# Kernel tuning notes

Measured on AMD Instinct MI355X. Metric: run time of the kernel, lower is better.

## Reference

```python
import jax, jax.numpy as jnp
import numpy as np

HIDDEN = 4096
RANK = 4
DELTA = 1.0
BATCH = 4096


def glorot(key, shape):
    return jax.random.uniform(key, shape, minval=-1.0, maxval=1.0) * jnp.sqrt(2.0 / sum(shape))


def setup_inputs() -> dict:
    key = jax.random.key(0)
    k1, k2, k3, k4, k5, k6 = jax.random.split(key, 6)
    return {
        "h": jax.random.normal(k5, (BATCH, HIDDEN), dtype=jnp.float32),
        "x": jax.random.normal(k6, (BATCH, HIDDEN), dtype=jnp.float32),
        "a_diag": glorot(k1, (HIDDEN,)),
        "p_vec": glorot(k2, (HIDDEN, RANK)),
        "q_vec": glorot(k3, (HIDDEN, RANK)),
        "b_mat": glorot(k4, (HIDDEN, HIDDEN)),
    }


def reference(h, x, a_diag, p_vec, q_vec, b_mat):
    # Per-sample original math: (I + delta*(diag(a) + p q^T)) @ h + delta * b_mat.T @ x
    # Batched (rows of h/x are samples) with the Woodbury-style low-rank form:
    #   A_disc @ h  ->  h + delta*(a*h + (h @ q) @ p^T)
    #   B_disc^T @ x -> delta * (x @ b_mat)
    Ah = h + DELTA * (h * a_diag + (h @ q_vec) @ p_vec.T)  # [B, N]
    Bx = DELTA * (x @ b_mat)                               # [B, N]
    return Ah + Bx
```

## Files before the change

### kernel.cpp

```cpp
#include <hip/hip_runtime.h>
#include <hip/hip_bf16.h>
#include <stdint.h>
#include <stddef.h>

#define HIDDEN 4096
#define BATCH  4096
#define RANK   4

typedef _Float16 f16;
typedef __attribute__((ext_vector_type(8))) _Float16 half8;
typedef __attribute__((ext_vector_type(4))) float f32x4;
typedef __attribute__((ext_vector_type(8))) unsigned short ushort8;

#define ASYNC_COPY16(g, l)                                                     \
  __builtin_amdgcn_global_load_lds(                                            \
      (__attribute__((address_space(1))) void*)(g),                            \
      (__attribute__((address_space(3))) void*)(l), 16, 0, 0)

__global__ void cast_f16_kernel(const float* __restrict__ src, f16* __restrict__ dst) {
  size_t i = ((size_t)blockIdx.x * blockDim.x + threadIdx.x) * 8;
  float4 v0 = *(const float4*)(src + i);
  float4 v1 = *(const float4*)(src + i + 4);
  union { f16 h[8]; ushort8 v; } u;
  u.h[0] = (f16)v0.x; u.h[1] = (f16)v0.y; u.h[2] = (f16)v0.z; u.h[3] = (f16)v0.w;
  u.h[4] = (f16)v1.x; u.h[5] = (f16)v1.y; u.h[6] = (f16)v1.z; u.h[7] = (f16)v1.w;
  *(ushort8*)(dst + i) = u.v;
}

__global__ void transpose_cast_kernel(const float* __restrict__ B, f16* __restrict__ Bt) {
  __shared__ f16 tile[64][80];
  const int t = threadIdx.x;
  const int bx = blockIdx.x;
  const int by = blockIdx.y;
  const int tx = t & 15, ty = t >> 4;
  #pragma unroll
  for (int i = 0; i < 4; i++) {
    int row = ty + i * 16;
    float4 v = *(const float4*)(B + (size_t)(by * 64 + row) * HIDDEN + bx * 64 + tx * 4);
    tile[tx * 4 + 0][row] = (f16)v.x;
    tile[tx * 4 + 1][row] = (f16)v.y;
    tile[tx * 4 + 2][row] = (f16)v.z;
    tile[tx * 4 + 3][row] = (f16)v.w;
  }
  __syncthreads();
  const int wx = t & 7, wy = t >> 3;
  #pragma unroll
  for (int i = 0; i < 2; i++) {
    int n = wy + i * 32;
    ushort8 v = *(ushort8*)&tile[n][wx * 8];
    *(ushort8*)(Bt + (size_t)(bx * 64 + n) * HIDDEN + by * 64 + wx * 8) = v;
  }
}

__global__ void hq_kernel(const float* __restrict__ h, const float* __restrict__ q,
                          float* __restrict__ hq) {
  const int b = blockIdx.x;
  const float* hrow = h + (size_t)b * HIDDEN;
  float a0 = 0.f, a1 = 0.f, a2 = 0.f, a3 = 0.f;
  for (int k = threadIdx.x; k < HIDDEN; k += 256) {
    float hv = hrow[k];
    float4 qv = *(const float4*)(q + (size_t)k * RANK);
    a0 += hv * qv.x; a1 += hv * qv.y; a2 += hv * qv.z; a3 += hv * qv.w;
  }
  #pragma unroll
  for (int off = 32; off; off >>= 1) {
    a0 += __shfl_down(a0, off, 64);
    a1 += __shfl_down(a1, off, 64);
    a2 += __shfl_down(a2, off, 64);
    a3 += __shfl_down(a3, off, 64);
  }
  __shared__ float red[4][4];
  const int wave = threadIdx.x >> 6, lane = threadIdx.x & 63;
  if (lane == 0) { red[wave][0] = a0; red[wave][1] = a1; red[wave][2] = a2; red[wave][3] = a3; }
  __syncthreads();
  if (threadIdx.x < 4) {
    float s = red[0][threadIdx.x] + red[1][threadIdx.x] + red[2][threadIdx.x] + red[3][threadIdx.x];
    hq[(size_t)b * RANK + threadIdx.x] = s;
  }
}

#define BM 128
#define BN 128
#define BK 64

__global__ __launch_bounds__(256) void gemm_fused_kernel(
    const f16* __restrict__ Xb, const f16* __restrict__ Bt,
    const float* __restrict__ h, const float* __restrict__ a_diag,
    const float* __restrict__ p_vec, const float* __restrict__ hq,
    float* __restrict__ out) {
  __shared__ f16 As[BM * BK];
  __shared__ f16 Bs[BN * BK];
  const int tid = threadIdx.x;
  const int bm = blockIdx.x, bn = blockIdx.y;
  const int wave = tid >> 6, lane = tid & 63;
  const int wm = wave & 1, wn = wave >> 1;

  const int srow = tid >> 3;
  const int sseg = (tid & 7) ^ (srow & 7);
  const f16* ag = Xb + (size_t)(bm * BM + srow) * HIDDEN + sseg * 8;
  const f16* bg = Bt + (size_t)(bn * BN + srow) * HIDDEN + sseg * 8;
  char* as_base = (char*)As + wave * 1024;
  char* bs_base = (char*)Bs + wave * 1024;
  const size_t rowblk = (size_t)32 * HIDDEN;

  f32x4 acc[4][4];
  #pragma unroll
  for (int i = 0; i < 4; i++)
    #pragma unroll
    for (int j = 0; j < 4; j++)
      acc[i][j] = (f32x4){0.f, 0.f, 0.f, 0.f};

  const int q = lane >> 4;
  const int fm = lane & 15;
  const int swz = lane & 7;

  for (int k0 = 0; k0 < HIDDEN; k0 += BK) {
    #pragma unroll
    for (int o = 0; o < 4; o++) {
      ASYNC_COPY16(ag + o * rowblk, as_base + o * 4096);
      ASYNC_COPY16(bg + o * rowblk, bs_base + o * 4096);
    }
    ag += BK; bg += BK;
    __syncthreads();

    #pragma unroll
    for (int kk = 0; kk < 2; kk++) {
      const int sa = ((kk << 2) | q) ^ swz;
      half8 af[4], bf[4];
      #pragma unroll
      for (int i = 0; i < 4; i++)
        af[i] = *(const half8*)(As + (wm * 64 + i * 16 + fm) * BK + sa * 8);
      #pragma unroll
      for (int j = 0; j < 4; j++)
        bf[j] = *(const half8*)(Bs + (wn * 64 + j * 16 + fm) * BK + sa * 8);
      #pragma unroll
      for (int i = 0; i < 4; i++)
        #pragma unroll
        for (int j = 0; j < 4; j++)
          acc[i][j] = __builtin_amdgcn_mfma_f32_16x16x32_f16(af[i], bf[j], acc[i][j], 0, 0, 0);
    }
    __syncthreads();
  }

  float ad[4];
  float4 pv[4];
  #pragma unroll
  for (int j = 0; j < 4; j++) {
    const int gn = bn * BN + wn * 64 + j * 16 + fm;
    ad[j] = 1.0f + a_diag[gn];
    pv[j] = *(const float4*)(p_vec + (size_t)gn * RANK);
  }
  #pragma unroll
  for (int i = 0; i < 4; i++) {
    #pragma unroll
    for (int r = 0; r < 4; r++) {
      const size_t gb = (size_t)(bm * BM + wm * 64 + i * 16 + q * 4 + r);
      const float4 hv = *(const float4*)(hq + gb * RANK);
      const size_t rowoff = gb * HIDDEN + bn * BN + wn * 64 + fm;
      #pragma unroll
      for (int j = 0; j < 4; j++) {
        const size_t idx = rowoff + j * 16;
        const float hval = __builtin_nontemporal_load(&h[idx]);
        const float v = acc[i][j][r] + hval * ad[j] +
                        hv.x * pv[j].x + hv.y * pv[j].y + hv.z * pv[j].z + hv.w * pv[j].w;
        __builtin_nontemporal_store(v, &out[idx]);
      }
    }
  }
}

__global__ void gemm_f32_fallback_kernel(const float* __restrict__ x, const float* __restrict__ bmat,
                                         const float* __restrict__ h, const float* __restrict__ a_diag,
                                         const float* __restrict__ p_vec, const float* __restrict__ hq,
                                         float* __restrict__ out) {
  __shared__ float As[16][64];
  __shared__ float Bs[16][68];
  const int t = threadIdx.x;
  const int bx = blockIdx.x, by = blockIdx.y;
  const int tm = t & 15, tn = t >> 4;
  float acc[4][4] = {{0.f}};
  for (int k0 = 0; k0 < HIDDEN; k0 += 16) {
    #pragma unroll
    for (int l = 0; l < 4; l++) {
      int idx = t + l * 256;
      int r = idx >> 4, k = idx & 15;
      As[k][r] = x[(size_t)(by * 64 + r) * HIDDEN + k0 + k];
      int kb = idx >> 6, nb = idx & 63;
      Bs[kb][nb] = bmat[(size_t)(k0 + kb) * HIDDEN + bx * 64 + nb];
    }
    __syncthreads();
    #pragma unroll
    for (int k = 0; k < 16; k++) {
      float av[4], bv[4];
      #pragma unroll
      for (int ii = 0; ii < 4; ii++) av[ii] = As[k][tm * 4 + ii];
      #pragma unroll
      for (int jj = 0; jj < 4; jj++) bv[jj] = Bs[k][tn * 4 + jj];
      #pragma unroll
      for (int ii = 0; ii < 4; ii++)
        #pragma unroll
        for (int jj = 0; jj < 4; jj++)
          acc[ii][jj] += av[ii] * bv[jj];
    }
    __syncthreads();
  }
  #pragma unroll
  for (int jj = 0; jj < 4; jj++) {
    int gn = bx * 64 + tn * 4 + jj;
    float ad = 1.0f + a_diag[gn];
    float4 pv = *(const float4*)(p_vec + (size_t)gn * RANK);
    #pragma unroll
    for (int ii = 0; ii < 4; ii++) {
      size_t gb = (size_t)(by * 64 + tm * 4 + ii);
      float4 hv = *(const float4*)(hq + gb * RANK);
      size_t idx = gb * HIDDEN + gn;
      out[idx] = acc[ii][jj] + h[idx] * ad +
                 hv.x * pv.x + hv.y * pv.y + hv.z * pv.z + hv.w * pv.w;
    }
  }
}

extern "C" void kernel_launch(void* const* d_in, const int* in_sizes, int n_in,
                              void* d_out, int out_size, void* d_ws, size_t ws_size,
                              hipStream_t stream) {
  const float* h      = (const float*)d_in[0];
  const float* x      = (const float*)d_in[1];
  const float* a_diag = (const float*)d_in[2];
  const float* p_vec  = (const float*)d_in[3];
  const float* q_vec  = (const float*)d_in[4];
  const float* b_mat  = (const float*)d_in[5];
  float* out = (float*)d_out;

  const size_t nElem = (size_t)BATCH * HIDDEN;
  const size_t hq_bytes = (size_t)BATCH * RANK * sizeof(float);
  const size_t need = hq_bytes + 2 * nElem * sizeof(f16);

  float* hq = (float*)d_ws;
  hq_kernel<<<BATCH, 256, 0, stream>>>(h, q_vec, hq);

  if (ws_size >= need) {
    f16* Xb = (f16*)((char*)d_ws + hq_bytes);
    f16* Bt = Xb + nElem;
    cast_f16_kernel<<<nElem / 2048, 256, 0, stream>>>(x, Xb);
    transpose_cast_kernel<<<dim3(HIDDEN / 64, HIDDEN / 64), 256, 0, stream>>>(b_mat, Bt);
    gemm_fused_kernel<<<dim3(BATCH / BM, HIDDEN / BN), 256, 0, stream>>>(
        Xb, Bt, h, a_diag, p_vec, hq, out);
  } else {
    gemm_f32_fallback_kernel<<<dim3(HIDDEN / 64, BATCH / 64), 256, 0, stream>>>(
        x, b_mat, h, a_diag, p_vec, hq, out);
  }
}
```

Before: 381.1 us.

## Fuse B transpose-cast, x cast and h@q into one prep kernel

Merges three preprocessing launches (hq reduction, x fp16 cast, B transpose+cast) into a single prep kernel whose blocks split by index between transposing B and processing one batch row. Row blocks read h and x together, cast x to fp16 and compute the rank-4 h@q product with vectorized loads. The B transpose tile is now kept as fp32 with padding to avoid LDS bank conflicts, and the cast happens on read-out. This removes two launch gaps and lets the independent prep work overlap within one grid.

New measurement: 382.5 us. About the same (+0.4%).

```diff
diff --git a/kernel.cpp b/kernel.cpp
--- a/kernel.cpp
+++ b/kernel.cpp
@@ -11,44 +11,86 @@
 typedef __attribute__((ext_vector_type(8))) _Float16 half8;
 typedef __attribute__((ext_vector_type(4))) float f32x4;
 typedef __attribute__((ext_vector_type(8))) unsigned short ushort8;
+typedef __attribute__((ext_vector_type(4))) unsigned short ushort4v;
 
 #define ASYNC_COPY16(g, l)                                                     \
   __builtin_amdgcn_global_load_lds(                                            \
       (__attribute__((address_space(1))) void*)(g),                            \
       (__attribute__((address_space(3))) void*)(l), 16, 0, 0)
 
-__global__ void cast_f16_kernel(const float* __restrict__ src, f16* __restrict__ dst) {
-  size_t i = ((size_t)blockIdx.x * blockDim.x + threadIdx.x) * 8;
-  float4 v0 = *(const float4*)(src + i);
-  float4 v1 = *(const float4*)(src + i + 4);
-  union { f16 h[8]; ushort8 v; } u;
-  u.h[0] = (f16)v0.x; u.h[1] = (f16)v0.y; u.h[2] = (f16)v0.z; u.h[3] = (f16)v0.w;
-  u.h[4] = (f16)v1.x; u.h[5] = (f16)v1.y; u.h[6] = (f16)v1.z; u.h[7] = (f16)v1.w;
-  *(ushort8*)(dst + i) = u.v;
-}
-
-__global__ void transpose_cast_kernel(const float* __restrict__ B, f16* __restrict__ Bt) {
-  __shared__ f16 tile[64][80];
+__global__ __launch_bounds__(256) void prep_kernel(
+    const float* __restrict__ B, f16* __restrict__ Bt,
+    const float* __restrict__ x, f16* __restrict__ Xb,
+    const float* __restrict__ h, const float* __restrict__ q,
+    float* __restrict__ hq) {
+  __shared__ float tile[64][65];
+  const int id = blockIdx.x;
   const int t = threadIdx.x;
-  const int bx = blockIdx.x;
-  const int by = blockIdx.y;
-  const int tx = t & 15, ty = t >> 4;
-  #pragma unroll
-  for (int i = 0; i < 4; i++) {
-    int row = ty + i * 16;
-    float4 v = *(const float4*)(B + (size_t)(by * 64 + row) * HIDDEN + bx * 64 + tx * 4);
-    tile[tx * 4 + 0][row] = (f16)v.x;
-    tile[tx * 4 + 1][row] = (f16)v.y;
-    tile[tx * 4 + 2][row] = (f16)v.z;
-    tile[tx * 4 + 3][row] = (f16)v.w;
-  }
-  __syncthreads();
-  const int wx = t & 7, wy = t >> 3;
-  #pragma unroll
-  for (int i = 0; i < 2; i++) {
-    int n = wy + i * 32;
-    ushort8 v = *(ushort8*)&tile[n][wx * 8];
-    *(ushort8*)(Bt + (size_t)(bx * 64 + n) * HIDDEN + by * 64 + wx * 8) = v;
+
+  if (id < 4096) {
+    const int bx = id & 63;
+    const int by = id >> 6;
+    const int tx = t & 15, ty = t >> 4;
+    #pragma unroll
+    for (int i = 0; i < 4; i++) {
+      const int row = ty + i * 16;
+      float4 v = *(const float4*)(B + (size_t)(by * 64 + row) * HIDDEN + bx * 64 + tx * 4);
+      tile[tx * 4 + 0][row] = v.x;
+      tile[tx * 4 + 1][row] = v.y;
+      tile[tx * 4 + 2][row] = v.z;
+      tile[tx * 4 + 3][row] = v.w;
+    }
+    __syncthreads();
+    const int wx = t & 7, wy = t >> 3;
+    #pragma unroll
+    for (int i = 0; i < 2; i++) {
+      const int n = wy + 32 * i;
+      union { f16 hh[8]; ushort8 v; } u;
+      #pragma unroll
+      for (int c = 0; c < 8; c++) u.hh[c] = (f16)tile[n][wx * 8 + c];
+      *(ushort8*)(Bt + (size_t)(bx * 64 + n) * HIDDEN + by * 64 + wx * 8) = u.v;
+    }
+  } else {
+    const int row = id - 4096;
+    const float* hrow = h + (size_t)row * HIDDEN;
+    const float* xrow = x + (size_t)row * HIDDEN;
+    f16* xbrow = Xb + (size_t)row * HIDDEN;
+    float a0 = 0.f, a1 = 0.f, a2 = 0.f, a3 = 0.f;
+    #pragma unroll
+    for (int c = 0; c < 4; c++) {
+      const int k = c * 1024 + t * 4;
+      const float4 hv = *(const float4*)(hrow + k);
+      const float4 xv = *(const float4*)(xrow + k);
+      union { f16 hh[4]; ushort4v v; } u;
+      u.hh[0] = (f16)xv.x; u.hh[1] = (f16)xv.y; u.hh[2] = (f16)xv.z; u.hh[3] = (f16)xv.w;
+      *(ushort4v*)(xbrow + k) = u.v;
+      const float4 q0 = *(const float4*)(q + (size_t)(k + 0) * RANK);
+      const float4 q1 = *(const float4*)(q + (size_t)(k + 1) * RANK);
+      const float4 q2 = *(const float4*)(q + (size_t)(k + 2) * RANK);
+      const float4 q3 = *(const float4*)(q + (size_t)(k + 3) * RANK);
+      a0 += hv.x * q0.x + hv.y * q1.x + hv.z * q2.x + hv.w * q3.x;
+      a1 += hv.x * q0.y + hv.y * q1.y + hv.z * q2.y + hv.w * q3.y;
+      a2 += hv.x * q0.z + hv.y * q1.z + hv.z * q2.z + hv.w * q3.z;
+      a3 += hv.x * q0.w + hv.y * q1.w + hv.z * q2.w + hv.w * q3.w;
+    }
+    #pragma unroll
+    for (int off = 32; off; off >>= 1) {
+      a0 += __shfl_down(a0, off, 64);
+      a1 += __shfl_down(a1, off, 64);
+      a2 += __shfl_down(a2, off, 64);
+      a3 += __shfl_down(a3, off, 64);
+    }
+    float* red = &tile[0][0];
+    const int wave = t >> 6, lane = t & 63;
+    if (lane == 0) {
+      red[wave * 4 + 0] = a0; red[wave * 4 + 1] = a1;
+      red[wave * 4 + 2] = a2; red[wave * 4 + 3] = a3;
+    }
+    __syncthreads();
+    if (t < 4) {
+      float s = red[0 + t] + red[4 + t] + red[8 + t] + red[12 + t];
+      hq[(size_t)row * RANK + t] = s;
+    }
   }
 }
 
@@ -236,16 +278,15 @@
   const size_t need = hq_bytes + 2 * nElem * sizeof(f16);
 
   float* hq = (float*)d_ws;
-  hq_kernel<<<BATCH, 256, 0, stream>>>(h, q_vec, hq);
 
   if (ws_size >= need) {
     f16* Xb = (f16*)((char*)d_ws + hq_bytes);
     f16* Bt = Xb + nElem;
-    cast_f16_kernel<<<nElem / 2048, 256, 0, stream>>>(x, Xb);
-    transpose_cast_kernel<<<dim3(HIDDEN / 64, HIDDEN / 64), 256, 0, stream>>>(b_mat, Bt);
+    prep_kernel<<<4096 + BATCH, 256, 0, stream>>>(b_mat, Bt, x, Xb, h, q_vec, hq);
     gemm_fused_kernel<<<dim3(BATCH / BM, HIDDEN / BN), 256, 0, stream>>>(
         Xb, Bt, h, a_diag, p_vec, hq, out);
   } else {
+    hq_kernel<<<BATCH, 256, 0, stream>>>(h, q_vec, hq);
     gemm_f32_fallback_kernel<<<dim3(HIDDEN / 64, BATCH / 64), 256, 0, stream>>>(
         x, b_mat, h, a_diag, p_vec, hq, out);
   }
```
